# Kernel tuning notes

Hardware: AMD Instinct MI355X
Metric: run time of the kernel (lower is better)

The kernel has to match this reference:

```python
import jax, jax.numpy as jnp
import numpy as np

N_NODES = 50000
N_EDGES = 1600000
IN_F = 256
OUT_F = 128
N_REL = 500
NEG_SLOPE = 0.2
EPS = 1e-10


def setup_inputs() -> dict:
    key = jax.random.key(0)
    ks = jax.random.split(key, 7)
    h = jax.random.normal(ks[0], (N_NODES, IN_F), dtype=jnp.float32)
    rows = jax.random.randint(ks[1], (N_EDGES,), 0, N_NODES)
    cols = jax.random.randint(ks[2], (N_EDGES,), 0, N_NODES)
    edge_types = jax.random.randint(ks[3], (N_EDGES,), 0, N_REL)
    # learned params (xavier-ish small scale)
    W = jax.random.normal(ks[4], (IN_F, OUT_F), dtype=jnp.float32) * 0.05
    rel_emb = jax.random.normal(ks[5], (N_REL, OUT_F), dtype=jnp.float32) * 0.05
    a = jax.random.normal(ks[6], (2 * OUT_F + OUT_F,), dtype=jnp.float32) * 0.05
    return {"h": h, "rows": rows, "cols": cols, "edge_types": edge_types,
            "W": W, "rel_emb": rel_emb, "a": a}


def reference(h, rows, cols, edge_types, W, rel_emb, a):
    N = h.shape[0]
    d = W.shape[1]
    Wh = h @ W                                   # [N, out]
    # a^T [Wh_i || Wh_j || r] decomposed to avoid materializing the concat
    a_i, a_j, a_r = a[:d], a[d:2 * d], a[2 * d:]
    s_node_i = Wh @ a_i                          # [N]
    s_node_j = Wh @ a_j                          # [N]
    s_rel = rel_emb @ a_r                        # [R]
    e = s_node_i[rows] + s_node_j[cols] + s_rel[edge_types]   # [E]
    e = jax.nn.leaky_relu(e, negative_slope=NEG_SLOPE)
    e = e - jnp.max(e)                           # global max-shift as in original
    exp_e = jnp.exp(e)
    sum_exp = jax.ops.segment_sum(exp_e, rows, num_segments=N)  # [N]
    alpha = exp_e / (sum_exp[rows] + EPS)        # [E]  (dropout is identity in eval)
    # sparse matmul: h'_i = sum_{j in N(i)} alpha_ij * Wh_j
    h_prime = jax.ops.segment_sum(alpha[:, None] * Wh[cols], rows, num_segments=N)
    return jax.nn.elu(h_prime)
```

## Files before the change

### kernel.cpp

```cpp
#include <hip/hip_runtime.h>

#define N_NODES 50000
#define N_EDGES 1600000
#define IN_F    256
#define OUT_F   128
#define N_REL   500
#define NEG_SLOPE 0.2f
#define EPS_F   1e-10f
#define GEMM_ROWS 64

#define NB       1563
#define CAP      1408
#define BIN_CHUNK 16384
#define NBIN_BLK 98

typedef __attribute__((ext_vector_type(8))) __bf16 bf16x8;
typedef __attribute__((ext_vector_type(4))) float f32x4;

static __device__ __forceinline__ float bf2f(unsigned short u) {
    unsigned v = ((unsigned)u) << 16;
    float f;
    __builtin_memcpy(&f, &v, 4);
    return f;
}
static __device__ __forceinline__ unsigned short f2bf(float f) {
    unsigned u;
    __builtin_memcpy(&u, &f, 4);
    unsigned rounding = 0x7fffu + ((u >> 16) & 1u);
    u += rounding;
    return (unsigned short)(u >> 16);
}

__global__ __launch_bounds__(256) void wconv_k(
    const float* __restrict__ W,
    const float* __restrict__ a,
    unsigned short* __restrict__ WbfT,
    float* __restrict__ wa_i, float* __restrict__ wa_j)
{
    __shared__ float ash[2 * OUT_F];
    int t = threadIdx.x;
    if (t < 2 * OUT_F) ash[t] = a[t];
    __syncthreads();
    float si = 0.f, sj = 0.f;
    #pragma unroll 4
    for (int n = 0; n < OUT_F; ++n) {
        float w = W[t * OUT_F + n];
        WbfT[n * IN_F + t] = f2bf(w);
        si += w * ash[n];
        sj += w * ash[OUT_F + n];
    }
    wa_i[t] = si;
    wa_j[t] = sj;
}

__global__ __launch_bounds__(256) void srel_k(
    const float* __restrict__ rel_emb,
    const float* __restrict__ a,
    float* __restrict__ s_rel)
{
    int rid  = blockIdx.x * 4 + (threadIdx.x >> 6);
    int lane = threadIdx.x & 63;
    if (rid >= N_REL) return;
    float2 re = *(const float2*)(rel_emb + (size_t)rid * OUT_F + 2 * lane);
    float2 ar = *(const float2*)(a + 2 * OUT_F + 2 * lane);
    float sr = re.x * ar.x + re.y * ar.y;
    #pragma unroll
    for (int off = 32; off; off >>= 1) sr += __shfl_xor(sr, off, 64);
    if (lane == 0) s_rel[rid] = sr;
}

__global__ __launch_bounds__(256) void gemm_wh(
    const float* __restrict__ h,
    const unsigned short* __restrict__ WbfT,
    const float* __restrict__ wa_i, const float* __restrict__ wa_j,
    unsigned short* __restrict__ Whb,
    float* __restrict__ s_i, float* __restrict__ s_j)
{
    __shared__ unsigned short Ash[GEMM_ROWS * IN_F];
    const int t    = threadIdx.x;
    const int wv   = t >> 6;
    const int lane = t & 63;
    const int quad = lane >> 4;
    const int l15  = lane & 15;
    const int r0   = blockIdx.x * GEMM_ROWS;

    bf16x8 Bfrag[2][8];
    #pragma unroll
    for (int ct2 = 0; ct2 < 2; ++ct2) {
        int n = 32 * wv + 16 * ct2 + l15;
        #pragma unroll
        for (int ks = 0; ks < 8; ++ks)
            Bfrag[ct2][ks] = *(const bf16x8*)(WbfT + (size_t)n * IN_F + 32 * ks + 8 * quad);
    }

    float4 wai = *(const float4*)(wa_i + lane * 4);
    float4 waj = *(const float4*)(wa_j + lane * 4);

    #pragma unroll
    for (int i = 0; i < 16; ++i) {
        int q   = t + 256 * i;
        int row = q >> 6;
        int k   = (q & 63) * 4;
        int gr  = r0 + row;
        float4 v = make_float4(0.f, 0.f, 0.f, 0.f);
        if (gr < N_NODES) v = *(const float4*)(h + (size_t)gr * IN_F + k);
        int ks = k >> 5, qd = (k >> 3) & 3, j = k & 7;
        int rg = row >> 4, m15 = row & 15;
        int off = ((((rg << 3) + ks) << 6) + ((qd << 4) | m15)) * 8 + j;
        ushort4 p;
        p.x = f2bf(v.x); p.y = f2bf(v.y); p.z = f2bf(v.z); p.w = f2bf(v.w);
        *(ushort4*)(Ash + off) = p;
        float si = v.x * wai.x + v.y * wai.y + v.z * wai.z + v.w * wai.w;
        float sj = v.x * waj.x + v.y * waj.y + v.z * waj.z + v.w * waj.w;
        #pragma unroll
        for (int o = 32; o; o >>= 1) {
            si += __shfl_xor(si, o, 64);
            sj += __shfl_xor(sj, o, 64);
        }
        if (lane == 0 && gr < N_NODES) { s_i[gr] = si; s_j[gr] = sj; }
    }
    __syncthreads();

    #pragma unroll 1
    for (int rg = 0; rg < 4; ++rg) {
        const unsigned short* base = Ash + (((rg << 3) << 6) + lane) * 8;
        bf16x8 Afrag[8];
        #pragma unroll
        for (int ks = 0; ks < 8; ++ks)
            Afrag[ks] = *(const bf16x8*)(base + (ks << 6) * 8);
        f32x4 acc0 = {0.f, 0.f, 0.f, 0.f};
        f32x4 acc1 = {0.f, 0.f, 0.f, 0.f};
        #pragma unroll
        for (int ks = 0; ks < 8; ++ks) {
            acc0 = __builtin_amdgcn_mfma_f32_16x16x32_bf16(Afrag[ks], Bfrag[0][ks], acc0, 0, 0, 0);
            acc1 = __builtin_amdgcn_mfma_f32_16x16x32_bf16(Afrag[ks], Bfrag[1][ks], acc1, 0, 0, 0);
        }
        #pragma unroll
        for (int reg = 0; reg < 4; ++reg) {
            int gr = r0 + 16 * rg + quad * 4 + reg;
            if (gr < N_NODES) {
                Whb[(size_t)gr * OUT_F + 32 * wv + l15]      = f2bf(acc0[reg]);
                Whb[(size_t)gr * OUT_F + 32 * wv + 16 + l15] = f2bf(acc1[reg]);
            }
        }
    }
}

__global__ __launch_bounds__(1024) void bin_k(
    const int* __restrict__ rows, const int* __restrict__ cols, const int* __restrict__ types,
    const float* __restrict__ s_i, const float* __restrict__ s_j, const float* __restrict__ s_rel,
    int* __restrict__ cnt, uint2* __restrict__ epk)
{
    __shared__ int hist[NB];
    __shared__ int lbase[NB];
    __shared__ int cur[NB];
    int t = threadIdx.x;
    for (int i = t; i < NB; i += 1024) { hist[i] = 0; cur[i] = 0; }
    __syncthreads();

    int base = blockIdx.x * BIN_CHUNK;
    float cw[16];
    unsigned cm[16];
    #pragma unroll
    for (int i = 0; i < 16; ++i) {
        int e = base + t + 1024 * i;
        if (e < N_EDGES) {
            int r = rows[e], c = cols[e], ty = types[e];
            float v = s_i[r] + s_j[c] + s_rel[ty];
            v = (v > 0.f) ? v : NEG_SLOPE * v;
            cw[i] = __expf(v);
            int b = r >> 5;
            cm[i] = (unsigned)c | ((unsigned)(r & 31) << 16) | ((unsigned)b << 21);
            atomicAdd(&hist[b], 1);
        } else {
            cw[i] = 0.f;
            cm[i] = 0xffffffffu;
        }
    }
    __syncthreads();
    for (int i = t; i < NB; i += 1024)
        if (hist[i] > 0) lbase[i] = atomicAdd(&cnt[i], hist[i]);
    __syncthreads();
    #pragma unroll
    for (int i = 0; i < 16; ++i) {
        int e = base + t + 1024 * i;
        if (e < N_EDGES) {
            int b = cm[i] >> 21;
            int loc = lbase[b] + atomicAdd(&cur[b], 1);
            if (loc < CAP)
                epk[(size_t)b * CAP + loc] = make_uint2(__float_as_uint(cw[i]), cm[i] & 0x1fffffu);
        }
    }
}

__global__ __launch_bounds__(256) void bucket_agg(
    const int* __restrict__ cnt, const uint2* __restrict__ epk,
    const unsigned short* __restrict__ Whb,
    float* __restrict__ out)
{
    __shared__ uint2 sorted[CAP];
    __shared__ int hist[32];
    __shared__ int offs[33];
    __shared__ int cur[32];

    const int t    = threadIdx.x;
    const int wid  = t >> 6;
    const int lane = t & 63;
    const int b    = blockIdx.x;
    const int n    = min(cnt[b], CAP);
    const uint2* ep = epk + (size_t)b * CAP;
    const unsigned* Whu = (const unsigned*)Whb;

    if (t < 32) { hist[t] = 0; }
    __syncthreads();

    uint2 rec[6];
    #pragma unroll
    for (int i = 0; i < 6; ++i) {
        int idx = t + 256 * i;
        rec[i] = (idx < n) ? ep[idx] : make_uint2(0u, 0xffffffffu);
    }
    #pragma unroll
    for (int i = 0; i < 6; ++i)
        if (rec[i].y != 0xffffffffu) atomicAdd(&hist[(rec[i].y >> 16) & 31], 1);
    __syncthreads();
    if (wid == 0 && lane < 32) {
        int v = hist[lane];
        #pragma unroll
        for (int off = 1; off < 32; off <<= 1) {
            int u = __shfl_up(v, off, 64);
            if (lane >= off) v += u;
        }
        offs[lane + 1] = v;
        if (lane == 0) offs[0] = 0;
        cur[lane] = v - hist[lane];
    }
    __syncthreads();
    #pragma unroll
    for (int i = 0; i < 6; ++i) {
        if (rec[i].y != 0xffffffffu) {
            int pos = atomicAdd(&cur[(rec[i].y >> 16) & 31], 1);
            sorted[pos] = rec[i];
        }
    }
    __syncthreads();

    #pragma unroll 1
    for (int rl = 0; rl < 8; ++rl) {
        int row = wid * 8 + rl;
        int i = offs[row], e1 = offs[row + 1];
        float s = 0.f, x0 = 0.f, x1 = 0.f;
        for (; i + 8 <= e1; i += 8) {
            uint2 rc[8];
            #pragma unroll
            for (int j = 0; j < 8; ++j) rc[j] = sorted[i + j];
            unsigned p[8];
            #pragma unroll
            for (int j = 0; j < 8; ++j)
                p[j] = Whu[(size_t)(rc[j].y & 0xffffu) * 64 + lane];
            #pragma unroll
            for (int j = 0; j < 8; ++j) {
                float w = __uint_as_float(rc[j].x);
                s  += w;
                x0 += w * bf2f(p[j] & 0xffffu);
                x1 += w * bf2f(p[j] >> 16);
            }
        }
        for (; i + 4 <= e1; i += 4) {
            uint2 r0 = sorted[i], r1 = sorted[i + 1], r2 = sorted[i + 2], r3 = sorted[i + 3];
            unsigned p0 = Whu[(size_t)(r0.y & 0xffffu) * 64 + lane];
            unsigned p1 = Whu[(size_t)(r1.y & 0xffffu) * 64 + lane];
            unsigned p2 = Whu[(size_t)(r2.y & 0xffffu) * 64 + lane];
            unsigned p3 = Whu[(size_t)(r3.y & 0xffffu) * 64 + lane];
            float w0 = __uint_as_float(r0.x), w1 = __uint_as_float(r1.x);
            float w2 = __uint_as_float(r2.x), w3 = __uint_as_float(r3.x);
            s  += (w0 + w1) + (w2 + w3);
            x0 += w0 * bf2f(p0 & 0xffffu) + w1 * bf2f(p1 & 0xffffu)
                + w2 * bf2f(p2 & 0xffffu) + w3 * bf2f(p3 & 0xffffu);
            x1 += w0 * bf2f(p0 >> 16) + w1 * bf2f(p1 >> 16)
                + w2 * bf2f(p2 >> 16) + w3 * bf2f(p3 >> 16);
        }
        for (; i < e1; ++i) {
            uint2 r0 = sorted[i];
            unsigned p0 = Whu[(size_t)(r0.y & 0xffffu) * 64 + lane];
            float w0 = __uint_as_float(r0.x);
            s  += w0;
            x0 += w0 * bf2f(p0 & 0xffffu);
            x1 += w0 * bf2f(p0 >> 16);
        }
        int grow = b * 32 + row;
        if (grow < N_NODES) {
            float inv = 1.f / (s + EPS_F);
            float v0 = x0 * inv, v1 = x1 * inv;
            v0 = (v0 > 0.f) ? v0 : (__expf(v0) - 1.f);
            v1 = (v1 > 0.f) ? v1 : (__expf(v1) - 1.f);
            *(float2*)(out + (size_t)grow * OUT_F + 2 * lane) = make_float2(v0, v1);
        }
    }
}

extern "C" void kernel_launch(void* const* d_in, const int* in_sizes, int n_in,
                              void* d_out, int out_size, void* d_ws, size_t ws_size,
                              hipStream_t stream)
{
    const float* h     = (const float*)d_in[0];
    const int*   rows  = (const int*)d_in[1];
    const int*   cols  = (const int*)d_in[2];
    const int*   types = (const int*)d_in[3];
    const float* W     = (const float*)d_in[4];
    const float* rel   = (const float*)d_in[5];
    const float* a     = (const float*)d_in[6];

    char* ws = (char*)d_ws;
    size_t off = 0;
    auto alloc = [&](size_t bytes) -> void* {
        void* p = ws + off;
        off = (off + bytes + 255) & ~(size_t)255;
        return p;
    };
    unsigned short* Whb  = (unsigned short*)alloc((size_t)N_NODES * OUT_F * 2);
    unsigned short* WbfT = (unsigned short*)alloc((size_t)IN_F * OUT_F * 2);
    float* wa_i   = (float*)alloc((size_t)IN_F * 4);
    float* wa_j   = (float*)alloc((size_t)IN_F * 4);
    float* s_i    = (float*)alloc((size_t)N_NODES * 4);
    float* s_j    = (float*)alloc((size_t)N_NODES * 4);
    float* s_rel  = (float*)alloc((size_t)N_REL * 4);
    int*   cnt    = (int*)alloc((size_t)NB * 4);
    uint2* epk    = (uint2*)alloc((size_t)NB * CAP * 8);
    (void)ws_size; (void)in_sizes; (void)n_in; (void)out_size;

    hipMemsetAsync(cnt, 0, (size_t)NB * 4, stream);

    wconv_k<<<1, 256, 0, stream>>>(W, a, WbfT, wa_i, wa_j);
    srel_k<<<(N_REL + 3) / 4, 256, 0, stream>>>(rel, a, s_rel);
    gemm_wh<<<(N_NODES + GEMM_ROWS - 1) / GEMM_ROWS, 256, 0, stream>>>(
        h, WbfT, wa_i, wa_j, Whb, s_i, s_j);
    bin_k<<<NBIN_BLK, 1024, 0, stream>>>(rows, cols, types, s_i, s_j, s_rel, cnt, epk);
    bucket_agg<<<NB, 256, 0, stream>>>(cnt, epk, Whb, (float*)d_out);
}
```

Before: 249.0 us.

## Parallelize W conversion, compute node scores via MFMA, shrink bin blocks, cache s_rel

The single-block W conversion becomes a 64-block kernel using wave reductions, and the folded attention vectors are stored as bf16. The per-row shuffle reductions for s_i/s_j in the GEMM are replaced by an extra MFMA on wave 0 against a sparse bf16 fragment, so the scores now come from bf16-rounded h. The binning kernel moves from 98 blocks of 1024 threads to 391 blocks of 256 threads with s_rel cached in LDS, for better occupancy and less global traffic. The bf16 scores lower precision and may shift the softmax weights.

Result: faster. 222.1 us (-10.8%).

```diff
diff --git a/kernel.cpp b/kernel.cpp
--- a/kernel.cpp
+++ b/kernel.cpp
@@ -11,8 +11,8 @@
 
 #define NB       1563
 #define CAP      1408
-#define BIN_CHUNK 16384
-#define NBIN_BLK 98
+#define BIN_CHUNK 4096
+#define NBIN_BLK 391
 
 typedef __attribute__((ext_vector_type(8))) __bf16 bf16x8;
 typedef __attribute__((ext_vector_type(4))) float f32x4;
@@ -35,22 +35,23 @@
     const float* __restrict__ W,
     const float* __restrict__ a,
     unsigned short* __restrict__ WbfT,
-    float* __restrict__ wa_i, float* __restrict__ wa_j)
-{
-    __shared__ float ash[2 * OUT_F];
-    int t = threadIdx.x;
-    if (t < 2 * OUT_F) ash[t] = a[t];
-    __syncthreads();
-    float si = 0.f, sj = 0.f;
-    #pragma unroll 4
-    for (int n = 0; n < OUT_F; ++n) {
-        float w = W[t * OUT_F + n];
-        WbfT[n * IN_F + t] = f2bf(w);
-        si += w * ash[n];
-        sj += w * ash[OUT_F + n];
-    }
-    wa_i[t] = si;
-    wa_j[t] = sj;
+    unsigned short* __restrict__ wai_bf, unsigned short* __restrict__ waj_bf)
+{
+    int wid  = threadIdx.x >> 6;
+    int lane = threadIdx.x & 63;
+    int k    = blockIdx.x * 4 + wid;
+    int n0   = lane * 2;
+    float2 wv2 = *(const float2*)(W + (size_t)k * OUT_F + n0);
+    WbfT[(size_t)n0 * IN_F + k]       = f2bf(wv2.x);
+    WbfT[(size_t)(n0 + 1) * IN_F + k] = f2bf(wv2.y);
+    float si = wv2.x * a[n0] + wv2.y * a[n0 + 1];
+    float sj = wv2.x * a[OUT_F + n0] + wv2.y * a[OUT_F + n0 + 1];
+    #pragma unroll
+    for (int off = 32; off; off >>= 1) {
+        si += __shfl_xor(si, off, 64);
+        sj += __shfl_xor(sj, off, 64);
+    }
+    if (lane == 0) { wai_bf[k] = f2bf(si); waj_bf[k] = f2bf(sj); }
 }
 
 __global__ __launch_bounds__(256) void srel_k(
@@ -72,7 +73,7 @@
 __global__ __launch_bounds__(256) void gemm_wh(
     const float* __restrict__ h,
     const unsigned short* __restrict__ WbfT,
-    const float* __restrict__ wa_i, const float* __restrict__ wa_j,
+    const unsigned short* __restrict__ wai_bf, const unsigned short* __restrict__ waj_bf,
     unsigned short* __restrict__ Whb,
     float* __restrict__ s_i, float* __restrict__ s_j)
 {
@@ -92,9 +93,15 @@
         for (int ks = 0; ks < 8; ++ks)
             Bfrag[ct2][ks] = *(const bf16x8*)(WbfT + (size_t)n * IN_F + 32 * ks + 8 * quad);
     }
-
-    float4 wai = *(const float4*)(wa_i + lane * 4);
-    float4 waj = *(const float4*)(wa_j + lane * 4);
+    bf16x8 Sfrag[8];
+    if (wv == 0) {
+        const unsigned short* ssrc = (l15 == 0) ? wai_bf : waj_bf;
+        #pragma unroll
+        for (int ks = 0; ks < 8; ++ks) {
+            if (l15 < 2) Sfrag[ks] = *(const bf16x8*)(ssrc + 32 * ks + 8 * quad);
+            else         Sfrag[ks] = (bf16x8)(__bf16)0.0f;
+        }
+    }
 
     #pragma unroll
     for (int i = 0; i < 16; ++i) {
@@ -110,14 +117,6 @@
         ushort4 p;
         p.x = f2bf(v.x); p.y = f2bf(v.y); p.z = f2bf(v.z); p.w = f2bf(v.w);
         *(ushort4*)(Ash + off) = p;
-        float si = v.x * wai.x + v.y * wai.y + v.z * wai.z + v.w * wai.w;
-        float sj = v.x * waj.x + v.y * waj.y + v.z * waj.z + v.w * waj.w;
-        #pragma unroll
-        for (int o = 32; o; o >>= 1) {
-            si += __shfl_xor(si, o, 64);
-            sj += __shfl_xor(sj, o, 64);
-        }
-        if (lane == 0 && gr < N_NODES) { s_i[gr] = si; s_j[gr] = sj; }
     }
     __syncthreads();
 
@@ -143,10 +142,24 @@
                 Whb[(size_t)gr * OUT_F + 32 * wv + 16 + l15] = f2bf(acc1[reg]);
             }
         }
-    }
-}
-
-__global__ __launch_bounds__(1024) void bin_k(
+        if (wv == 0) {
+            f32x4 acc2 = {0.f, 0.f, 0.f, 0.f};
+            #pragma unroll
+            for (int ks = 0; ks < 8; ++ks)
+                acc2 = __builtin_amdgcn_mfma_f32_16x16x32_bf16(Afrag[ks], Sfrag[ks], acc2, 0, 0, 0);
+            #pragma unroll
+            for (int reg = 0; reg < 4; ++reg) {
+                int gr = r0 + 16 * rg + quad * 4 + reg;
+                if (gr < N_NODES) {
+                    if (l15 == 0) s_i[gr] = acc2[reg];
+                    else if (l15 == 1) s_j[gr] = acc2[reg];
+                }
+            }
+        }
+    }
+}
+
+__global__ __launch_bounds__(256) void bin_k(
     const int* __restrict__ rows, const int* __restrict__ cols, const int* __restrict__ types,
     const float* __restrict__ s_i, const float* __restrict__ s_j, const float* __restrict__ s_rel,
     int* __restrict__ cnt, uint2* __restrict__ epk)
@@ -154,8 +167,10 @@
     __shared__ int hist[NB];
     __shared__ int lbase[NB];
     __shared__ int cur[NB];
+    __shared__ float srl[N_REL];
     int t = threadIdx.x;
-    for (int i = t; i < NB; i += 1024) { hist[i] = 0; cur[i] = 0; }
+    for (int i = t; i < NB; i += 256) { hist[i] = 0; cur[i] = 0; }
+    for (int i = t; i < N_REL; i += 256) srl[i] = s_rel[i];
     __syncthreads();
 
     int base = blockIdx.x * BIN_CHUNK;
@@ -163,10 +178,10 @@
     unsigned cm[16];
     #pragma unroll
     for (int i = 0; i < 16; ++i) {
-        int e = base + t + 1024 * i;
+        int e = base + t + 256 * i;
         if (e < N_EDGES) {
             int r = rows[e], c = cols[e], ty = types[e];
-            float v = s_i[r] + s_j[c] + s_rel[ty];
+            float v = s_i[r] + s_j[c] + srl[ty];
             v = (v > 0.f) ? v : NEG_SLOPE * v;
             cw[i] = __expf(v);
             int b = r >> 5;
@@ -178,12 +193,12 @@
         }
     }
     __syncthreads();
-    for (int i = t; i < NB; i += 1024)
+    for (int i = t; i < NB; i += 256)
         if (hist[i] > 0) lbase[i] = atomicAdd(&cnt[i], hist[i]);
     __syncthreads();
     #pragma unroll
     for (int i = 0; i < 16; ++i) {
-        int e = base + t + 1024 * i;
+        int e = base + t + 256 * i;
         if (e < N_EDGES) {
             int b = cm[i] >> 21;
             int loc = lbase[b] + atomicAdd(&cur[b], 1);
@@ -318,10 +333,10 @@
         off = (off + bytes + 255) & ~(size_t)255;
         return p;
     };
-    unsigned short* Whb  = (unsigned short*)alloc((size_t)N_NODES * OUT_F * 2);
-    unsigned short* WbfT = (unsigned short*)alloc((size_t)IN_F * OUT_F * 2);
-    float* wa_i   = (float*)alloc((size_t)IN_F * 4);
-    float* wa_j   = (float*)alloc((size_t)IN_F * 4);
+    unsigned short* Whb   = (unsigned short*)alloc((size_t)N_NODES * OUT_F * 2);
+    unsigned short* WbfT  = (unsigned short*)alloc((size_t)IN_F * OUT_F * 2);
+    unsigned short* wai_bf = (unsigned short*)alloc((size_t)IN_F * 2);
+    unsigned short* waj_bf = (unsigned short*)alloc((size_t)IN_F * 2);
     float* s_i    = (float*)alloc((size_t)N_NODES * 4);
     float* s_j    = (float*)alloc((size_t)N_NODES * 4);
     float* s_rel  = (float*)alloc((size_t)N_REL * 4);
@@ -331,10 +346,10 @@
 
     hipMemsetAsync(cnt, 0, (size_t)NB * 4, stream);
 
-    wconv_k<<<1, 256, 0, stream>>>(W, a, WbfT, wa_i, wa_j);
+    wconv_k<<<64, 256, 0, stream>>>(W, a, WbfT, wai_bf, waj_bf);
     srel_k<<<(N_REL + 3) / 4, 256, 0, stream>>>(rel, a, s_rel);
     gemm_wh<<<(N_NODES + GEMM_ROWS - 1) / GEMM_ROWS, 256, 0, stream>>>(
-        h, WbfT, wa_i, wa_j, Whb, s_i, s_j);
-    bin_k<<<NBIN_BLK, 1024, 0, stream>>>(rows, cols, types, s_i, s_j, s_rel, cnt, epk);
+        h, WbfT, wai_bf, waj_bf, Whb, s_i, s_j);
+    bin_k<<<NBIN_BLK, 256, 0, stream>>>(rows, cols, types, s_i, s_j, s_rel, cnt, epk);
     bucket_agg<<<NB, 256, 0, stream>>>(cnt, epk, Whb, (float*)d_out);
 }
```
